# Performance work log

Hardware: AMD Instinct MI355X
Metric: run time of the kernel (lower is better)

The kernel has to match this reference:

```python
import jax, jax.numpy as jnp
import numpy as np

IGNORE_INDEX = -100
FIXED_TAG_WEIGHT = 2.0
ALLOWED_TOKEN_WEIGHT = 1.5


def setup_inputs() -> dict:
    key = jax.random.key(0)
    k1, k2 = jax.random.split(key)
    B, S, V = 2, 2048, 32000
    logits = jax.random.normal(k1, (B, S, V), dtype=jnp.float32)
    # small id range so tag subsequence matches actually occur
    labels = jax.random.randint(k2, (B, S), 0, 20).astype(jnp.int64)
    tag0 = jnp.array([5, 6, 7], dtype=jnp.int64)       # e.g. tokenizer.encode('<think>')
    tag1 = jnp.array([10, 11], dtype=jnp.int64)        # e.g. tokenizer.encode('</think>')
    allowed_ids = jnp.array([3, 4], dtype=jnp.int64)   # single allowed color token ids
    return {"logits": logits, "labels": labels, "tag0": tag0, "tag1": tag1,
            "allowed_ids": allowed_ids}


def _covered(labels, tag):
    """Boolean [B,S] mask of positions covered by any occurrence of `tag` in labels."""
    B, S = labels.shape
    L = tag.shape[0]          # static (concrete tag length)
    n = S - L + 1             # number of sliding windows
    match = jnp.ones((B, n), dtype=bool)
    for k in range(L):        # L is tiny (2-3); unrolled, fully vectorized over B,S
        match = match & (labels[:, k:k + n] == tag[k])
    cov = jnp.zeros((B, S), dtype=bool)
    for k in range(L):        # dilate match to cover the full tag span
        cov = cov | jnp.pad(match, ((0, 0), (k, L - 1 - k)))
    return cov


def reference(logits, labels, tag0, tag1, allowed_ids):
    B, S = labels.shape
    weights = jnp.ones((B, S), dtype=jnp.float32)
    # fixed tags first (fixed_tag_weight > 1.0)
    for tag in (tag0, tag1):
        weights = jnp.where(_covered(labels, tag), FIXED_TAG_WEIGHT, weights)
    # allowed single-token ids (allowed_token_weight > 1.0), applied after, may overwrite
    allowed_hit = jnp.any(labels[..., None] == allowed_ids, axis=-1)
    weights = jnp.where(allowed_hit, ALLOWED_TOKEN_WEIGHT, weights)

    # ForCausalLMLoss: shift, CE with ignore_index=-100, mean over valid tokens
    shift_logits = logits[:, :-1, :]            # [B, S-1, V]
    shift_labels = labels[:, 1:]                # [B, S-1]
    logp = jax.nn.log_softmax(shift_logits, axis=-1)
    nll = -jnp.take_along_axis(logp, jnp.clip(shift_labels, 0)[..., None], axis=-1)[..., 0]
    valid = (shift_labels != IGNORE_INDEX).astype(nll.dtype)
    ce = jnp.sum(nll * valid) / jnp.maximum(jnp.sum(valid), 1.0)
    # torch code: (scalar_loss * weights.view(-1)).mean() == scalar_loss * weights.mean()
    return ce * jnp.mean(weights)
```

## Files before the change

### kernel.cpp

```cpp
#include <hip/hip_runtime.h>
#include <math.h>

static constexpr int kB = 2;
static constexpr int kS = 2048;
static constexpr int kV = 32000;
static constexpr int kIgnore = -100;
static constexpr float kTagW = 2.0f;
static constexpr float kAllowW = 1.5f;


__global__ __launch_bounds__(256) void row_nll_kernel(
    const float* __restrict__ logits, const int* __restrict__ labels,
    float* __restrict__ ws) {
  const int row = blockIdx.x;
  const int b = row / (kS - 1);
  const int s = row - b * (kS - 1);
  const float* __restrict__ rowp = logits + (size_t)(b * kS + s) * kV;
  const float4* __restrict__ row4 = (const float4*)rowp;
  const int tid = threadIdx.x;

  float l0 = 0.f, l1 = 0.f, l2 = 0.f, l3 = 0.f;
  int i = tid;
  for (; i + 768 < kV / 4; i += 1024) {
    float4 a = row4[i];
    float4 c = row4[i + 256];
    float4 d = row4[i + 512];
    float4 e = row4[i + 768];
    l0 += __expf(a.x) + __expf(a.y) + __expf(a.z) + __expf(a.w);
    l1 += __expf(c.x) + __expf(c.y) + __expf(c.z) + __expf(c.w);
    l2 += __expf(d.x) + __expf(d.y) + __expf(d.z) + __expf(d.w);
    l3 += __expf(e.x) + __expf(e.y) + __expf(e.z) + __expf(e.w);
  }
  for (; i < kV / 4; i += 256) {
    float4 a = row4[i];
    l0 += __expf(a.x) + __expf(a.y) + __expf(a.z) + __expf(a.w);
  }
  float l = (l0 + l1) + (l2 + l3);

  for (int off = 32; off > 0; off >>= 1) l += __shfl_down(l, off, 64);

  __shared__ float sl[4];
  if ((tid & 63) == 0) sl[tid >> 6] = l;
  __syncthreads();

  if (tid == 0) {
    l = (sl[0] + sl[1]) + (sl[2] + sl[3]);
    const int lbl = labels[b * kS + s + 1];
    if (lbl != kIgnore) {
      const int c = lbl < 0 ? 0 : lbl;
      const float nll = __logf(l) - rowp[c];
      atomicAdd(&ws[0], nll);
      atomicAdd(&ws[1], 1.0f);
    }
  }
}

__device__ __forceinline__ bool covered_by(const int* __restrict__ lab, int s,
                                           const int* __restrict__ tag, int L) {
  bool cov = false;
  for (int k = 0; k < L; ++k) {
    const int st = s - k;
    if (st < 0 || st + L > kS) continue;
    bool match = true;
    for (int j = 0; j < L; ++j) match &= (lab[st + j] == tag[j]);
    cov |= match;
  }
  return cov;
}

__global__ __launch_bounds__(256) void weights_finalize_kernel(
    const int* __restrict__ labels,
    const int* __restrict__ tag0, int L0,
    const int* __restrict__ tag1, int L1,
    const int* __restrict__ allowed, int nA,
    const float* __restrict__ ws, float* __restrict__ out) {
  __shared__ int t0[16], t1[16], al[16];
  if (threadIdx.x < L0) t0[threadIdx.x] = tag0[threadIdx.x];
  if (threadIdx.x < L1) t1[threadIdx.x] = tag1[threadIdx.x];
  if (threadIdx.x < nA) al[threadIdx.x] = allowed[threadIdx.x];
  __syncthreads();

  float sum = 0.0f;
  for (int idx = threadIdx.x; idx < kB * kS; idx += 256) {
    const int b = idx / kS;
    const int s = idx - b * kS;
    const int* __restrict__ lab = labels + b * kS;
    float w = 1.0f;
    if (covered_by(lab, s, t0, L0)) w = kTagW;
    if (covered_by(lab, s, t1, L1)) w = kTagW;
    const int me = lab[s];
    for (int a = 0; a < nA; ++a)
      if (me == al[a]) w = kAllowW;
    sum += w;
  }

  for (int off = 32; off > 0; off >>= 1) sum += __shfl_down(sum, off, 64);
  __shared__ float ps[4];
  if ((threadIdx.x & 63) == 0) ps[threadIdx.x >> 6] = sum;
  __syncthreads();
  if (threadIdx.x == 0) {
    const float wsum = (ps[0] + ps[1]) + (ps[2] + ps[3]);
    const float ce = ws[0] / fmaxf(ws[1], 1.0f);
    out[0] = ce * (wsum * (1.0f / (float)(kB * kS)));
  }
}

extern "C" void kernel_launch(void* const* d_in, const int* in_sizes, int n_in,
                              void* d_out, int out_size, void* d_ws, size_t ws_size,
                              hipStream_t stream) {
  const float* logits = (const float*)d_in[0];
  const int* labels  = (const int*)d_in[1];
  const int* tag0    = (const int*)d_in[2];
  const int* tag1    = (const int*)d_in[3];
  const int* allowed = (const int*)d_in[4];
  float* ws  = (float*)d_ws;
  float* out = (float*)d_out;

  hipMemsetAsync(ws, 0, 2 * sizeof(float), stream);

  row_nll_kernel<<<kB * (kS - 1), 256, 0, stream>>>(logits, labels, ws);
  weights_finalize_kernel<<<1, 256, 0, stream>>>(labels, tag0, in_sizes[2],
                                                 tag1, in_sizes[3],
                                                 allowed, in_sizes[4], ws, out);
}
```

Before: 736.5 us.

## Deepen load batching with nontemporal loads and drop atomics and memset

The row log-sum-exp loop now issues eight nontemporal 16-byte loads per thread before any exp work, with a masked tail, so more memory requests are in flight and the streamed logits bypass cache retention. Per-row NLL values go into a workspace array instead of global atomics. The finalize kernel sums them along with the valid count, which also removes the memset launch. The single-block finalize now reads about 4K extra floats, and the larger register footprint may lower occupancy.

```diff
diff --git a/kernel.cpp b/kernel.cpp
--- a/kernel.cpp
+++ b/kernel.cpp
@@ -7,6 +7,9 @@
 static constexpr int kIgnore = -100;
 static constexpr float kTagW = 2.0f;
 static constexpr float kAllowW = 1.5f;
+static constexpr int kRows = kB * (kS - 1);
+
+typedef float vf4 __attribute__((ext_vector_type(4)));
 
 
 __global__ __launch_bounds__(256) void row_nll_kernel(
@@ -16,26 +19,40 @@
   const int b = row / (kS - 1);
   const int s = row - b * (kS - 1);
   const float* __restrict__ rowp = logits + (size_t)(b * kS + s) * kV;
-  const float4* __restrict__ row4 = (const float4*)rowp;
+  const vf4* __restrict__ row4 = (const vf4*)rowp;
   const int tid = threadIdx.x;
 
-  float l0 = 0.f, l1 = 0.f, l2 = 0.f, l3 = 0.f;
-  int i = tid;
-  for (; i + 768 < kV / 4; i += 1024) {
-    float4 a = row4[i];
-    float4 c = row4[i + 256];
-    float4 d = row4[i + 512];
-    float4 e = row4[i + 768];
-    l0 += __expf(a.x) + __expf(a.y) + __expf(a.z) + __expf(a.w);
-    l1 += __expf(c.x) + __expf(c.y) + __expf(c.z) + __expf(c.w);
-    l2 += __expf(d.x) + __expf(d.y) + __expf(d.z) + __expf(d.w);
-    l3 += __expf(e.x) + __expf(e.y) + __expf(e.z) + __expf(e.w);
+  float acc[8] = {0.f, 0.f, 0.f, 0.f, 0.f, 0.f, 0.f, 0.f};
+
+  for (int o = 0; o < 3; ++o) {
+    const int base = tid + o * 2048;
+    vf4 v[8];
+#pragma unroll
+    for (int u = 0; u < 8; ++u)
+      v[u] = __builtin_nontemporal_load(row4 + base + u * 256);
+#pragma unroll
+    for (int u = 0; u < 8; ++u)
+      acc[u] += __expf(v[u].x) + __expf(v[u].y) + __expf(v[u].z) + __expf(v[u].w);
   }
-  for (; i < kV / 4; i += 256) {
-    float4 a = row4[i];
-    l0 += __expf(a.x) + __expf(a.y) + __expf(a.z) + __expf(a.w);
+  {
+    const int base = tid + 6144;
+    vf4 v[8];
+#pragma unroll
+    for (int u = 0; u < 8; ++u) {
+      const int idx = base + u * 256;
+      v[u] = __builtin_nontemporal_load(row4 + (idx < 8000 ? idx : 0));
+    }
+#pragma unroll
+    for (int u = 0; u < 8; ++u) {
+      const int idx = base + u * 256;
+      const float e =
+          __expf(v[u].x) + __expf(v[u].y) + __expf(v[u].z) + __expf(v[u].w);
+      acc[u] += (idx < 8000) ? e : 0.0f;
+    }
   }
-  float l = (l0 + l1) + (l2 + l3);
+
+  float l = ((acc[0] + acc[1]) + (acc[2] + acc[3])) +
+            ((acc[4] + acc[5]) + (acc[6] + acc[7]));
 
   for (int off = 32; off > 0; off >>= 1) l += __shfl_down(l, off, 64);
 
@@ -46,12 +63,8 @@
   if (tid == 0) {
     l = (sl[0] + sl[1]) + (sl[2] + sl[3]);
     const int lbl = labels[b * kS + s + 1];
-    if (lbl != kIgnore) {
-      const int c = lbl < 0 ? 0 : lbl;
-      const float nll = __logf(l) - rowp[c];
-      atomicAdd(&ws[0], nll);
-      atomicAdd(&ws[1], 1.0f);
-    }
+    const int c = lbl < 0 ? 0 : lbl;
+    ws[row] = __logf(l) - rowp[c];
   }
 }
 
@@ -80,7 +93,7 @@
   if (threadIdx.x < nA) al[threadIdx.x] = allowed[threadIdx.x];
   __syncthreads();
 
-  float sum = 0.0f;
+  float wsum = 0.0f;
   for (int idx = threadIdx.x; idx < kB * kS; idx += 256) {
     const int b = idx / kS;
     const int s = idx - b * kS;
@@ -91,17 +104,36 @@
     const int me = lab[s];
     for (int a = 0; a < nA; ++a)
       if (me == al[a]) w = kAllowW;
-    sum += w;
+    wsum += w;
   }
 
-  for (int off = 32; off > 0; off >>= 1) sum += __shfl_down(sum, off, 64);
-  __shared__ float ps[4];
-  if ((threadIdx.x & 63) == 0) ps[threadIdx.x >> 6] = sum;
+  float nsum = 0.0f, vcnt = 0.0f;
+  for (int r = threadIdx.x; r < kRows; r += 256) {
+    const int b = r / (kS - 1);
+    const int s = r - b * (kS - 1);
+    if (labels[b * kS + s + 1] != kIgnore) {
+      nsum += ws[r];
+      vcnt += 1.0f;
+    }
+  }
+
+  for (int off = 32; off > 0; off >>= 1) {
+    wsum += __shfl_down(wsum, off, 64);
+    nsum += __shfl_down(nsum, off, 64);
+    vcnt += __shfl_down(vcnt, off, 64);
+  }
+  __shared__ float pw[4], pn[4], pv[4];
+  if ((threadIdx.x & 63) == 0) {
+    pw[threadIdx.x >> 6] = wsum;
+    pn[threadIdx.x >> 6] = nsum;
+    pv[threadIdx.x >> 6] = vcnt;
+  }
   __syncthreads();
   if (threadIdx.x == 0) {
-    const float wsum = (ps[0] + ps[1]) + (ps[2] + ps[3]);
-    const float ce = ws[0] / fmaxf(ws[1], 1.0f);
-    out[0] = ce * (wsum * (1.0f / (float)(kB * kS)));
+    const float W = (pw[0] + pw[1]) + (pw[2] + pw[3]);
+    const float N = (pn[0] + pn[1]) + (pn[2] + pn[3]);
+    const float V = (pv[0] + pv[1]) + (pv[2] + pv[3]);
+    out[0] = (N / fmaxf(V, 1.0f)) * (W * (1.0f / (float)(kB * kS)));
   }
 }
 
@@ -116,9 +148,7 @@
   float* ws  = (float*)d_ws;
   float* out = (float*)d_out;
 
-  hipMemsetAsync(ws, 0, 2 * sizeof(float), stream);
-
-  row_nll_kernel<<<kB * (kS - 1), 256, 0, stream>>>(logits, labels, ws);
+  row_nll_kernel<<<kRows, 256, 0, stream>>>(logits, labels, ws);
   weights_finalize_kernel<<<1, 256, 0, stream>>>(labels, tag0, in_sizes[2],
                                                  tag1, in_sizes[3],
                                                  allowed, in_sizes[4], ws, out);
```

Measured after the change: 658.4 us. -10.6%, faster.
